# Kernel optimization log

Hardware: AMD Instinct MI355X
Metric: run time of the kernel (lower is better)

Reference implementation:

```python
import jax, jax.numpy as jnp
import numpy as np

NEG_SLOPE = 0.2  # PyG GATConv leaky_relu slope
EPS = 1e-16


def gat_layer(x, W, att_src, att_dst, bias, src, dst, num_nodes, heads, out_c, concat):
    # x: [N, F_in], W: [F_in, heads*out_c], att_*: [heads, out_c], bias: [heads*out_c] or [out_c]
    xp = (x @ W).reshape(num_nodes, heads, out_c)              # [N, H, C]
    a_src = (xp * att_src).sum(-1)                             # [N, H]
    a_dst = (xp * att_dst).sum(-1)                             # [N, H]
    alpha = jax.nn.leaky_relu(a_src[src] + a_dst[dst], NEG_SLOPE)  # [E, H]
    # segment softmax over destination-node neighborhoods
    m = jax.ops.segment_max(alpha, dst, num_segments=num_nodes)   # [N, H]
    e = jnp.exp(alpha - m[dst])
    s = jax.ops.segment_sum(e, dst, num_segments=num_nodes)
    alpha = e / (s[dst] + EPS)                                 # [E, H]
    out = jax.ops.segment_sum(xp[src] * alpha[:, :, None], dst, num_segments=num_nodes)  # [N, H, C]
    out = out.reshape(num_nodes, heads * out_c) if concat else out.mean(axis=1)
    return out + bias


def setup_inputs() -> dict:
    key = jax.random.key(0)
    N, E, F = 100000, 3200000, 128
    ks = jax.random.split(key, 10)
    x = jax.random.normal(ks[0], (N, F), dtype=jnp.float32)
    edge_index = jax.random.randint(ks[1], (2, E), 0, N, dtype=jnp.int64)
    s1 = 1.0 / np.sqrt(F)
    W1 = jax.random.normal(ks[2], (F, 2 * 16), dtype=jnp.float32) * s1
    att_src1 = jax.random.normal(ks[3], (2, 16), dtype=jnp.float32) * 0.25
    att_dst1 = jax.random.normal(ks[4], (2, 16), dtype=jnp.float32) * 0.25
    b1 = jnp.zeros((32,), dtype=jnp.float32)
    W2 = jax.random.normal(ks[5], (32, 1), dtype=jnp.float32) * (1.0 / np.sqrt(32))
    att_src2 = jax.random.normal(ks[6], (1, 1), dtype=jnp.float32)
    att_dst2 = jax.random.normal(ks[7], (1, 1), dtype=jnp.float32)
    b2 = jnp.zeros((1,), dtype=jnp.float32)
    return {"x": x, "edge_index": edge_index, "W1": W1, "att_src1": att_src1,
            "att_dst1": att_dst1, "b1": b1, "W2": W2, "att_src2": att_src2,
            "att_dst2": att_dst2, "b2": b2}


def reference(x, edge_index, W1, att_src1, att_dst1, b1, W2, att_src2, att_dst2, b2):
    N = x.shape[0]
    # PyG GATConv adds self-loops by default
    loops = jnp.arange(N, dtype=edge_index.dtype)
    src = jnp.concatenate([edge_index[0], loops])
    dst = jnp.concatenate([edge_index[1], loops])
    h = gat_layer(x, W1, att_src1, att_dst1, b1, src, dst, N, 2, 16, True)   # [N, 32]
    h = jax.nn.relu(h)
    out = gat_layer(h, W2, att_src2, att_dst2, b2, src, dst, N, 1, 1, False)  # [N, 1]
    return out.sum(axis=0, keepdims=True)  # [1, 1]
```

## Files before the change

### kernel.cpp

```cpp
#include <hip/hip_runtime.h>
#include <hip/hip_bf16.h>
#include <hip/hip_fp16.h>
#include <hip/hip_fp8.h>
#include <math.h>

#define NEG_SLOPE 0.2f
#define EPS 1e-16f
#define CHUNK 4096
#define BSH 8
#define BNODES 256

__device__ __forceinline__ float leaky(float x) {
    return x > 0.f ? x : NEG_SLOPE * x;
}

__global__ __launch_bounds__(1024) void chunkhist_kernel(
    const int* __restrict__ ei, int E, int ET, int NB, int NC,
    int* __restrict__ cnt) {
    __shared__ int histL[1024];
    int t = threadIdx.x;
    int c = blockIdx.x;
    if (t < NB) histL[t] = 0;
    __syncthreads();
    int e0 = c * CHUNK;
#pragma unroll 4
    for (int i = t; i < CHUNK; i += 1024) {
        int e = e0 + i;
        if (e < ET) {
            int d = (e < E) ? ei[E + e] : (e - E);
            atomicAdd(&histL[d >> BSH], 1);
        }
    }
    __syncthreads();
    if (t < NB) cnt[(size_t)t * NC + c] = histL[t];
}

__global__ void scan_block(const int* __restrict__ in, int* __restrict__ out,
                           int* __restrict__ partials, int n) {
    __shared__ int tmp[1024];
    int t = threadIdx.x;
    int g = blockIdx.x * 1024 + t;
    int v = (g < n) ? in[g] : 0;
    tmp[t] = v;
    __syncthreads();
    for (int off = 1; off < 1024; off <<= 1) {
        int add = (t >= off) ? tmp[t - off] : 0;
        __syncthreads();
        tmp[t] += add;
        __syncthreads();
    }
    if (g < n) out[g] = tmp[t] - v;
    if (t == 1023) partials[blockIdx.x] = tmp[1023];
}

__global__ void scan_partials(int* __restrict__ partials, int P) {
    __shared__ int tmp[1024];
    int t = threadIdx.x;
    int v = (t < P) ? partials[t] : 0;
    tmp[t] = v;
    __syncthreads();
    for (int off = 1; off < 1024; off <<= 1) {
        int add = (t >= off) ? tmp[t - off] : 0;
        __syncthreads();
        tmp[t] += add;
        __syncthreads();
    }
    if (t < P) partials[t] = tmp[t] - v;
}

__device__ __forceinline__ int gscan(const int* scanned, const int* partials,
                                     size_t g) {
    return scanned[g] + partials[g >> 10];
}

__global__ __launch_bounds__(1024) void packsort_kernel(
    const int* __restrict__ ei, int E, int ET, int NB, int NC,
    const int* __restrict__ scanned, const int* __restrict__ partials,
    unsigned int* __restrict__ packed) {
    __shared__ unsigned int sortedL[CHUNK];
    __shared__ int gposL[CHUNK];
    __shared__ int histL[1024];
    __shared__ int tmpL[1024];
    __shared__ int cursorL[1024];
    __shared__ int diffL[1024];
    int t = threadIdx.x;
    int c = blockIdx.x;
    int e0 = c * CHUNK;
    int cw = ET - e0; if (cw > CHUNK) cw = CHUNK;

    if (t < NB) histL[t] = 0;
    __syncthreads();

    unsigned int pk[4]; int bb[4];
#pragma unroll
    for (int k = 0; k < 4; k++) {
        int i = t + k * 1024;
        bb[k] = -1;
        if (i < cw) {
            int e = e0 + i;
            int s, d;
            if (e < E) { s = ei[e]; d = ei[E + e]; } else { s = d = e - E; }
            bb[k] = d >> BSH;
            pk[k] = ((unsigned int)s << BSH) | (unsigned int)(d & (BNODES - 1));
            atomicAdd(&histL[bb[k]], 1);
        }
    }
    __syncthreads();
    int hv = (t < NB) ? histL[t] : 0;
    tmpL[t] = hv;
    __syncthreads();
    for (int off = 1; off < 1024; off <<= 1) {
        int add = (t >= off) ? tmpL[t - off] : 0;
        __syncthreads();
        tmpL[t] += add;
        __syncthreads();
    }
    if (t < NB) {
        int loff = tmpL[t] - hv;
        cursorL[t] = loff;
        size_t g = (size_t)t * NC + c;
        diffL[t] = gscan(scanned, partials, g) - loff;
    }
    __syncthreads();
#pragma unroll
    for (int k = 0; k < 4; k++) {
        if (bb[k] >= 0) {
            int lpos = atomicAdd(&cursorL[bb[k]], 1);
            sortedL[lpos] = pk[k];
            gposL[lpos] = diffL[bb[k]] + lpos;
        }
    }
    __syncthreads();
    for (int i = t; i < cw; i += 1024)
        packed[gposL[i]] = sortedL[i];
}

__global__ __launch_bounds__(1024) void localsort_kernel(
    const unsigned int* __restrict__ packed, const int* __restrict__ scanned,
    const int* __restrict__ partials, int NB, int NC, int ET,
    int* __restrict__ srt, int* __restrict__ binptr, int N) {
    __shared__ int histL[BNODES];
    __shared__ int offL[BNODES];
    __shared__ int curL[BNODES];
    int t = threadIdx.x;
    int bkt = blockIdx.x;
    int base = bkt * BNODES;
    int ebeg = gscan(scanned, partials, (size_t)bkt * NC);
    int eend = (bkt + 1 < NB) ? gscan(scanned, partials, (size_t)(bkt + 1) * NC) : ET;
    if (t < BNODES) histL[t] = 0;
    __syncthreads();
    for (int i = ebeg + t; i < eend; i += 1024)
        atomicAdd(&histL[packed[i] & (BNODES - 1)], 1);
    __syncthreads();
    if (t < BNODES) offL[t] = histL[t];
    __syncthreads();
    for (int off = 1; off < BNODES; off <<= 1) {
        int add = (t >= off && t < BNODES) ? offL[t - off] : 0;
        __syncthreads();
        if (t < BNODES) offL[t] += add;
        __syncthreads();
    }
    if (t < BNODES) {
        int ex = offL[t] - histL[t];
        curL[t] = ex;
        int gn = base + t;
        if (gn < N) binptr[gn] = ebeg + ex;
    }
    if (bkt == 0 && t == 0) binptr[N] = ET;
    __syncthreads();
    for (int i = ebeg + t; i < eend; i += 1024) {
        unsigned int p = packed[i];
        int dl = p & (BNODES - 1);
        int pos = ebeg + atomicAdd(&curL[dl], 1);
        srt[pos] = (int)(p >> BSH);
    }
}

__device__ __forceinline__ void fma4(float4& acc, float sc, const float4& wv) {
    acc.x = fmaf(sc, wv.x, acc.x);
    acc.y = fmaf(sc, wv.y, acc.y);
    acc.z = fmaf(sc, wv.z, acc.z);
    acc.w = fmaf(sc, wv.w, acc.w);
}

__global__ __launch_bounds__(256) void gemm1_kernel(
    const float* __restrict__ x, const float* __restrict__ W1,
    const float4* __restrict__ att_src4, const float4* __restrict__ att_dst4,
    unsigned int* __restrict__ xp1u, float* __restrict__ a_src,
    float* __restrict__ a_dst, int N) {
    __shared__ float4 wS4[128 * 8];
    __shared__ float4 xS4[64 * 32];
    int t = threadIdx.x;
    int base = blockIdx.x * 64;
#pragma unroll
    for (int i = 0; i < 4; i++)
        wS4[t + i * 256] = ((const float4*)W1)[t + i * 256];
#pragma unroll
    for (int i = 0; i < 8; i++) {
        int idx = t + i * 256;
        int row = idx >> 5, kb = idx & 31;
        xS4[idx] = (base + row < N) ? ((const float4*)x)[(size_t)(base + row) * 32 + kb]
                                    : make_float4(0.f, 0.f, 0.f, 0.f);
    }
    __syncthreads();

    int cq = t & 7;
    int rg = t >> 3;
    const float4* xr0 = xS4 + (rg * 2) * 32;
    const float4* xr1 = xr0 + 32;
    float4 a0 = make_float4(0.f, 0.f, 0.f, 0.f);
    float4 a1 = make_float4(0.f, 0.f, 0.f, 0.f);
#pragma unroll 4
    for (int kb = 0; kb < 32; kb++) {
        float4 x0 = xr0[kb];
        float4 x1 = xr1[kb];
        float4 w0 = wS4[(kb * 4 + 0) * 8 + cq];
        float4 w1 = wS4[(kb * 4 + 1) * 8 + cq];
        float4 w2 = wS4[(kb * 4 + 2) * 8 + cq];
        float4 w3 = wS4[(kb * 4 + 3) * 8 + cq];
        fma4(a0, x0.x, w0); fma4(a0, x0.y, w1); fma4(a0, x0.z, w2); fma4(a0, x0.w, w3);
        fma4(a1, x1.x, w0); fma4(a1, x1.y, w1); fma4(a1, x1.z, w2); fma4(a1, x1.w, w3);
    }

    float4 asv = att_src4[cq];
    float4 adv = att_dst4[cq];
    int r0 = base + rg * 2, r1 = r0 + 1;
    float va0 = a0.x * asv.x + a0.y * asv.y + a0.z * asv.z + a0.w * asv.w;
    float vd0 = a0.x * adv.x + a0.y * adv.y + a0.z * adv.z + a0.w * adv.w;
    float va1 = a1.x * asv.x + a1.y * asv.y + a1.z * asv.z + a1.w * asv.w;
    float vd1 = a1.x * adv.x + a1.y * adv.y + a1.z * adv.z + a1.w * adv.w;
#pragma unroll
    for (int off = 1; off <= 2; off <<= 1) {
        va0 += __shfl_xor(va0, off);
        vd0 += __shfl_xor(vd0, off);
        va1 += __shfl_xor(va1, off);
        vd1 += __shfl_xor(vd1, off);
    }
    if (r0 < N) {
        __hip_fp8x4_e4m3 q0(a0);
        xp1u[(size_t)r0 * 8 + cq] = *(unsigned int*)&q0;
        if ((cq & 3) == 0) {
            int h = cq >> 2;
            a_src[r0 * 2 + h] = va0;
            a_dst[r0 * 2 + h] = vd0;
        }
    }
    if (r1 < N) {
        __hip_fp8x4_e4m3 q1(a1);
        xp1u[(size_t)r1 * 8 + cq] = *(unsigned int*)&q1;
        if ((cq & 3) == 0) {
            int h = cq >> 2;
            a_src[r1 * 2 + h] = va1;
            a_dst[r1 * 2 + h] = vd1;
        }
    }
}

__global__ __launch_bounds__(256) void agg1_kernel(
    const int* __restrict__ binptr, const int* __restrict__ srt,
    const float2* __restrict__ a_src2, const float2* __restrict__ a_dst2,
    const unsigned char* __restrict__ xp1f8, const float* __restrict__ b1,
    const float* __restrict__ W2, float* __restrict__ xp2, int N) {
    int tg = blockIdx.x * blockDim.x + threadIdx.x;
    int n = tg >> 6;
    int lane = threadIdx.x & 63;
    if (n >= N) return;
    int eg = lane >> 3;
    int cq = lane & 7;
    int hsel = cq >> 2;
    int beg = binptr[n], end = binptr[n + 1];
    float2 ad = a_dst2[n];
    const unsigned char* xpb = xp1f8 + cq * 4;

    float acc0 = 0.f, acc1 = 0.f, acc2 = 0.f, acc3 = 0.f, ssum = 0.f;
    for (int i0 = beg; i0 < end; i0 += 64) {
        int cw = end - i0;
        if (cw > 64) cw = 64;
        int s_l = 0;
        unsigned int pk_l = 0u;
        if (lane < cw) {
            s_l = srt[i0 + lane];
            float2 as = a_src2[s_l];
            float e0 = __expf(leaky(as.x + ad.x));
            float e1 = __expf(leaky(as.y + ad.y));
            pk_l = ((__float_as_uint(e1) + 0x8000u) & 0xFFFF0000u) |
                   ((__float_as_uint(e0) + 0x8000u) >> 16);
        }
        int kmax = (cw + 7) >> 3;
#pragma unroll 2
        for (int k = 0; k < kmax; k++) {
            int es = k * 8 + eg;
            int sk = __shfl(s_l, es);
            unsigned int pw = (unsigned int)__shfl((int)pk_l, es);
            float ek = __uint_as_float(hsel ? (pw & 0xFFFF0000u) : (pw << 16));
            unsigned int u = *(const unsigned int*)(xpb + (size_t)sk * 32);
            float4 xv = (float4)(*reinterpret_cast<const __hip_fp8x4_e4m3*>(&u));
            acc0 = fmaf(ek, xv.x, acc0);
            acc1 = fmaf(ek, xv.y, acc1);
            acc2 = fmaf(ek, xv.z, acc2);
            acc3 = fmaf(ek, xv.w, acc3);
            ssum += ek;
        }
    }
#pragma unroll
    for (int off = 8; off <= 32; off <<= 1) {
        acc0 += __shfl_xor(acc0, off);
        acc1 += __shfl_xor(acc1, off);
        acc2 += __shfl_xor(acc2, off);
        acc3 += __shfl_xor(acc3, off);
        ssum += __shfl_xor(ssum, off);
    }
    float inv = 1.f / (ssum + EPS);
    int j0 = cq * 4;
    float p;
    {
        float hv0 = fmaxf(acc0 * inv + b1[j0 + 0], 0.f);
        float hv1 = fmaxf(acc1 * inv + b1[j0 + 1], 0.f);
        float hv2 = fmaxf(acc2 * inv + b1[j0 + 2], 0.f);
        float hv3 = fmaxf(acc3 * inv + b1[j0 + 3], 0.f);
        p = hv0 * W2[j0 + 0];
        p = fmaf(hv1, W2[j0 + 1], p);
        p = fmaf(hv2, W2[j0 + 2], p);
        p = fmaf(hv3, W2[j0 + 3], p);
    }
    p += __shfl_xor(p, 1);
    p += __shfl_xor(p, 2);
    p += __shfl_xor(p, 4);
    if (lane == 0) xp2[n] = p;
}

__global__ __launch_bounds__(256) void agg2_kernel(
    const int* __restrict__ binptr, const int* __restrict__ srt,
    const float* __restrict__ xp2, const float* __restrict__ as2p,
    const float* __restrict__ ad2p, const float* __restrict__ b2,
    float* __restrict__ partial, int N) {
    int slot = (blockIdx.x * blockDim.x + threadIdx.x) >> 5;
    int j = threadIdx.x & 31;
    int nslots = (gridDim.x * blockDim.x) >> 5;
    float as2 = as2p[0], ad2 = ad2p[0], bb = b2[0];
    float val = 0.f;
    for (int n = slot; n < N; n += nslots) {
        int beg = binptr[n], end = binptr[n + 1];
        float xd = xp2[n] * ad2;
        float se = 0.f, sa = 0.f;
        for (int i = beg + j; i < end; i += 32) {
            float xs = xp2[srt[i]];
            float ex = __expf(leaky(fmaf(xs, as2, xd)));
            se += ex;
            sa = fmaf(ex, xs, sa);
        }
#pragma unroll
        for (int off = 16; off >= 1; off >>= 1) {
            se += __shfl_xor(se, off);
            sa += __shfl_xor(sa, off);
        }
        if (j == 0) val += sa / (se + EPS) + bb;
    }
#pragma unroll
    for (int off = 32; off >= 1; off >>= 1) val += __shfl_xor(val, off);
    __shared__ float ls[4];
    int lane = threadIdx.x & 63, w = threadIdx.x >> 6;
    if (lane == 0) ls[w] = val;
    __syncthreads();
    if (threadIdx.x == 0) partial[blockIdx.x] = ls[0] + ls[1] + ls[2] + ls[3];
}

__global__ void final_reduce(const float* __restrict__ partial, float* __restrict__ out,
                             int P) {
    int t = threadIdx.x;
    float v = 0.f;
    for (int i = t; i < P; i += 1024) v += partial[i];
#pragma unroll
    for (int off = 32; off >= 1; off >>= 1) v += __shfl_xor(v, off);
    __shared__ float ls[16];
    int w = t >> 6, lane = t & 63;
    if (lane == 0) ls[w] = v;
    __syncthreads();
    if (t == 0) {
        float s = 0.f;
        for (int i = 0; i < 16; i++) s += ls[i];
        out[0] = s;
    }
}

extern "C" void kernel_launch(void* const* d_in, const int* in_sizes, int n_in,
                              void* d_out, int out_size, void* d_ws, size_t ws_size,
                              hipStream_t stream) {
    const float* x        = (const float*)d_in[0];
    const int*   ei       = (const int*)d_in[1];
    const float* W1       = (const float*)d_in[2];
    const float* att_src1 = (const float*)d_in[3];
    const float* att_dst1 = (const float*)d_in[4];
    const float* b1       = (const float*)d_in[5];
    const float* W2       = (const float*)d_in[6];
    const float* att_src2 = (const float*)d_in[7];
    const float* att_dst2 = (const float*)d_in[8];
    const float* b2       = (const float*)d_in[9];
    float* out = (float*)d_out;

    int N = in_sizes[0] / 128;
    int E = in_sizes[1] / 2;
    int ET = E + N;
    int NB = (N + BNODES - 1) / BNODES;
    int NC = (ET + CHUNK - 1) / CHUNK;
    int n_scan = NB * NC;
    int nb2 = (n_scan + 1023) / 1024;
    const int AGG2_BLOCKS = 2048;

    char* w = (char*)d_ws;
    unsigned char* xp1f8 = (unsigned char*)w; w += (size_t)N * 32;
    float* a_src   = (float*)w;  w += sizeof(float) * (size_t)N * 2;
    float* a_dst   = (float*)w;  w += sizeof(float) * (size_t)N * 2;
    float* xp2     = (float*)w;  w += sizeof(float) * (size_t)N;
    int* cnt       = (int*)w;    w += sizeof(int) * (size_t)n_scan;
    int* scanned   = (int*)w;    w += sizeof(int) * (size_t)(n_scan + 4);
    int* partials  = (int*)w;    w += sizeof(int) * 1024;
    float* part2   = (float*)w;  w += sizeof(float) * (size_t)AGG2_BLOCKS;
    unsigned int* packed = (unsigned int*)w; w += sizeof(unsigned int) * (size_t)ET;
    int* srt       = (int*)w;    w += sizeof(int) * (size_t)ET;
    int* binptr    = (int*)w;    w += sizeof(int) * (size_t)(N + 1);

    gemm1_kernel<<<(N + 63) / 64, 256, 0, stream>>>(x, W1,
                                                    (const float4*)att_src1,
                                                    (const float4*)att_dst1,
                                                    (unsigned int*)xp1f8, a_src,
                                                    a_dst, N);
    chunkhist_kernel<<<NC, 1024, 0, stream>>>(ei, E, ET, NB, NC, cnt);
    scan_block<<<nb2, 1024, 0, stream>>>(cnt, scanned, partials, n_scan);
    scan_partials<<<1, 1024, 0, stream>>>(partials, nb2);
    packsort_kernel<<<NC, 1024, 0, stream>>>(ei, E, ET, NB, NC, scanned, partials,
                                             packed);
    localsort_kernel<<<NB, 1024, 0, stream>>>(packed, scanned, partials, NB, NC, ET,
                                              srt, binptr, N);
    agg1_kernel<<<(N * 64 + 255) / 256, 256, 0, stream>>>(binptr, srt,
                                                          (const float2*)a_src,
                                                          (const float2*)a_dst,
                                                          xp1f8, b1, W2, xp2, N);
    agg2_kernel<<<AGG2_BLOCKS, 256, 0, stream>>>(binptr, srt, xp2,
                                                 att_src2, att_dst2, b2, part2, N);
    final_reduce<<<1, 1024, 0, stream>>>(part2, out, AGG2_BLOCKS);
}
```

Before: 164.1 us.

## Simplify agg1 edge loop, replace final reduce with atomic accumulation

agg1 no longer stages source indices and bf16-packed exp weights through a 64-wide chunk with shuffles. Each lane group now loads its own edge index, the per-head attention score and the fp8 features directly, and recomputes the exponent per lane. Memory-level parallelism should improve through unroll 4, at the cost of redundant srt/a_src loads and exp work across the 8 lanes of each edge. agg2 now atomically adds block partials into the output, which is zeroed by a memset, so the final_reduce launch is dropped. The agg2 grid is also doubled.

```diff
diff --git a/kernel.cpp b/kernel.cpp
--- a/kernel.cpp
+++ b/kernel.cpp
@@ -258,7 +258,7 @@
 
 __global__ __launch_bounds__(256) void agg1_kernel(
     const int* __restrict__ binptr, const int* __restrict__ srt,
-    const float2* __restrict__ a_src2, const float2* __restrict__ a_dst2,
+    const float* __restrict__ a_srcF, const float* __restrict__ a_dstF,
     const unsigned char* __restrict__ xp1f8, const float* __restrict__ b1,
     const float* __restrict__ W2, float* __restrict__ xp2, int N) {
     int tg = blockIdx.x * blockDim.x + threadIdx.x;
@@ -269,38 +269,28 @@
     int cq = lane & 7;
     int hsel = cq >> 2;
     int beg = binptr[n], end = binptr[n + 1];
-    float2 ad = a_dst2[n];
+    float adh = a_dstF[n * 2 + hsel];
     const unsigned char* xpb = xp1f8 + cq * 4;
+    const float* ash = a_srcF + hsel;
 
     float acc0 = 0.f, acc1 = 0.f, acc2 = 0.f, acc3 = 0.f, ssum = 0.f;
-    for (int i0 = beg; i0 < end; i0 += 64) {
-        int cw = end - i0;
-        if (cw > 64) cw = 64;
-        int s_l = 0;
-        unsigned int pk_l = 0u;
-        if (lane < cw) {
-            s_l = srt[i0 + lane];
-            float2 as = a_src2[s_l];
-            float e0 = __expf(leaky(as.x + ad.x));
-            float e1 = __expf(leaky(as.y + ad.y));
-            pk_l = ((__float_as_uint(e1) + 0x8000u) & 0xFFFF0000u) |
-                   ((__float_as_uint(e0) + 0x8000u) >> 16);
-        }
-        int kmax = (cw + 7) >> 3;
-#pragma unroll 2
-        for (int k = 0; k < kmax; k++) {
-            int es = k * 8 + eg;
-            int sk = __shfl(s_l, es);
-            unsigned int pw = (unsigned int)__shfl((int)pk_l, es);
-            float ek = __uint_as_float(hsel ? (pw & 0xFFFF0000u) : (pw << 16));
-            unsigned int u = *(const unsigned int*)(xpb + (size_t)sk * 32);
-            float4 xv = (float4)(*reinterpret_cast<const __hip_fp8x4_e4m3*>(&u));
-            acc0 = fmaf(ek, xv.x, acc0);
-            acc1 = fmaf(ek, xv.y, acc1);
-            acc2 = fmaf(ek, xv.z, acc2);
-            acc3 = fmaf(ek, xv.w, acc3);
-            ssum += ek;
-        }
+    int kmax = (end - beg + 7) >> 3;
+    int ib = beg + eg;
+#pragma unroll 4
+    for (int k = 0; k < kmax; k++) {
+        int idx = ib + k * 8;
+        bool valid = idx < end;
+        int s = srt[valid ? idx : beg];
+        float av = ash[s * 2];
+        unsigned int u = *(const unsigned int*)(xpb + (size_t)s * 32);
+        float ek = __expf(leaky(av + adh));
+        ek = valid ? ek : 0.f;
+        float4 xv = (float4)(*reinterpret_cast<const __hip_fp8x4_e4m3*>(&u));
+        acc0 = fmaf(ek, xv.x, acc0);
+        acc1 = fmaf(ek, xv.y, acc1);
+        acc2 = fmaf(ek, xv.z, acc2);
+        acc3 = fmaf(ek, xv.w, acc3);
+        ssum += ek;
     }
 #pragma unroll
     for (int off = 8; off <= 32; off <<= 1) {
@@ -333,7 +323,7 @@
     const int* __restrict__ binptr, const int* __restrict__ srt,
     const float* __restrict__ xp2, const float* __restrict__ as2p,
     const float* __restrict__ ad2p, const float* __restrict__ b2,
-    float* __restrict__ partial, int N) {
+    float* __restrict__ out, int N) {
     int slot = (blockIdx.x * blockDim.x + threadIdx.x) >> 5;
     int j = threadIdx.x & 31;
     int nslots = (gridDim.x * blockDim.x) >> 5;
@@ -362,25 +352,7 @@
     int lane = threadIdx.x & 63, w = threadIdx.x >> 6;
     if (lane == 0) ls[w] = val;
     __syncthreads();
-    if (threadIdx.x == 0) partial[blockIdx.x] = ls[0] + ls[1] + ls[2] + ls[3];
-}
-
-__global__ void final_reduce(const float* __restrict__ partial, float* __restrict__ out,
-                             int P) {
-    int t = threadIdx.x;
-    float v = 0.f;
-    for (int i = t; i < P; i += 1024) v += partial[i];
-#pragma unroll
-    for (int off = 32; off >= 1; off >>= 1) v += __shfl_xor(v, off);
-    __shared__ float ls[16];
-    int w = t >> 6, lane = t & 63;
-    if (lane == 0) ls[w] = v;
-    __syncthreads();
-    if (t == 0) {
-        float s = 0.f;
-        for (int i = 0; i < 16; i++) s += ls[i];
-        out[0] = s;
-    }
+    if (threadIdx.x == 0) atomicAdd(out, ls[0] + ls[1] + ls[2] + ls[3]);
 }
 
 extern "C" void kernel_launch(void* const* d_in, const int* in_sizes, int n_in,
@@ -405,7 +377,7 @@
     int NC = (ET + CHUNK - 1) / CHUNK;
     int n_scan = NB * NC;
     int nb2 = (n_scan + 1023) / 1024;
-    const int AGG2_BLOCKS = 2048;
+    const int AGG2_BLOCKS = 4096;
 
     char* w = (char*)d_ws;
     unsigned char* xp1f8 = (unsigned char*)w; w += (size_t)N * 32;
@@ -415,11 +387,11 @@
     int* cnt       = (int*)w;    w += sizeof(int) * (size_t)n_scan;
     int* scanned   = (int*)w;    w += sizeof(int) * (size_t)(n_scan + 4);
     int* partials  = (int*)w;    w += sizeof(int) * 1024;
-    float* part2   = (float*)w;  w += sizeof(float) * (size_t)AGG2_BLOCKS;
     unsigned int* packed = (unsigned int*)w; w += sizeof(unsigned int) * (size_t)ET;
     int* srt       = (int*)w;    w += sizeof(int) * (size_t)ET;
     int* binptr    = (int*)w;    w += sizeof(int) * (size_t)(N + 1);
 
+    hipMemsetAsync(out, 0, sizeof(float), stream);
     gemm1_kernel<<<(N + 63) / 64, 256, 0, stream>>>(x, W1,
                                                     (const float4*)att_src1,
                                                     (const float4*)att_dst1,
@@ -433,10 +405,8 @@
     localsort_kernel<<<NB, 1024, 0, stream>>>(packed, scanned, partials, NB, NC, ET,
                                               srt, binptr, N);
     agg1_kernel<<<(N * 64 + 255) / 256, 256, 0, stream>>>(binptr, srt,
-                                                          (const float2*)a_src,
-                                                          (const float2*)a_dst,
+                                                          a_src, a_dst,
                                                           xp1f8, b1, W2, xp2, N);
     agg2_kernel<<<AGG2_BLOCKS, 256, 0, stream>>>(binptr, srt, xp2,
-                                                 att_src2, att_dst2, b2, part2, N);
-    final_reduce<<<1, 1024, 0, stream>>>(part2, out, AGG2_BLOCKS);
-}
+                                                 att_src2, att_dst2, b2, out, N);
+}
```

After: 207.0 us. 1.26x slower.
